# Kernel tuning notes

Measured on AMD Instinct MI355X. Metric: run time of the kernel, lower is better.

The kernel has to match this reference:

```python
import jax, jax.numpy as jnp
import numpy as np

BITS = 4
QMAX = 2 ** (BITS - 1) - 1   # 7
OFF = 2 ** (BITS - 1)        # 8
L = 2 ** BITS                # 16 LUT levels per operand


def _quant(x):
    """Symmetric per-tensor quantization to signed BITS-bit levels.
    Returns integer-valued levels (as float, in [-OFF, QMAX]) and the scale."""
    s = jnp.maximum(jnp.max(jnp.abs(x)) / QMAX, 1e-8)
    q = jnp.clip(jnp.round(x / s), -OFF, QMAX)
    return q, s


def _lut_conv3x3(x, w, b, lut):
    """3x3 same-padding conv where every scalar multiply a*w is replaced by
    lut[idx(a), idx(w)]. x:[B,C,H,W], w:[O,C,3,3], b:[O], lut:[L,L]."""
    B, C, H, W = x.shape
    O = w.shape[0]
    qx, sx = _quant(x)
    qw, sw = _quant(w)
    # zero-padding: level 0 is the quantized value 0, so padding is exact
    xp = jnp.pad(qx, ((0, 0), (0, 0), (1, 1), (1, 1)))
    # im2col: [B, C, 9, H, W] -> [B, H, W, K], K = C*9 (order: c-major, then kh,kw)
    patches = jnp.stack([xp[:, :, i:i + H, j:j + W]
                         for i in range(3) for j in range(3)], axis=2)
    K = C * 9
    patches = patches.reshape(B, K, H, W).transpose(0, 2, 3, 1)
    idx_a = (patches + OFF).astype(jnp.int32)            # [B,H,W,K]
    mapped = lut[idx_a]                                   # [B,H,W,K,L]
    idx_w = (qw.reshape(O, K).T + OFF).astype(jnp.int32)  # [K,O]
    onehot_w = jax.nn.one_hot(idx_w, L, dtype=x.dtype)    # [K,O,L]
    # out[b,o,h,w] = sum_k lut[idx_a[b,h,w,k], idx_w[k,o]]
    out = jnp.einsum('bhwkl,kol->bohw', mapped, onehot_w)
    return out * (sx * sw) + b[None, :, None, None]


def _lut_linear(x, w, b, lut):
    """x:[B,F], w:[O,F], b:[O], lut:[L,L]; y[b,o]=sum_f lut[idx(x),idx(w)]."""
    qx, sx = _quant(x)
    qw, sw = _quant(w)
    idx_a = (qx + OFF).astype(jnp.int32)                 # [B,F]
    mapped = lut[idx_a]                                   # [B,F,L]
    idx_w = (qw.T + OFF).astype(jnp.int32)                # [F,O]
    onehot_w = jax.nn.one_hot(idx_w, L, dtype=x.dtype)    # [F,O,L]
    out = jnp.einsum('bfl,fol->bo', mapped, onehot_w)
    return out * (sx * sw) + b[None, :]


def _maxpool2(x):
    B, C, H, W = x.shape
    return x.reshape(B, C, H // 2, 2, W // 2, 2).max(axis=(3, 5))


def setup_inputs() -> dict:
    key = jax.random.key(0)
    ks = jax.random.split(key, 20)
    d = {}
    d['x'] = jax.random.normal(ks[0], (8, 3, 32, 32), jnp.float32)
    conv_shapes = [(64, 3), (192, 64), (384, 192), (256, 384), (256, 256)]
    for i, (o, c) in enumerate(conv_shapes):
        d[f'w{i}'] = jax.random.normal(ks[1 + 2 * i], (o, c, 3, 3), jnp.float32) * 0.05
        d[f'b{i}'] = jax.random.normal(ks[2 + 2 * i], (o,), jnp.float32) * 0.01
    fc_shapes = [(4096, 4096), (4096, 4096), (10, 4096)]
    for j, (o, f) in enumerate(fc_shapes):
        d[f'w{5 + j}'] = jax.random.normal(ks[11 + 2 * j], (o, f), jnp.float32) * 0.02
        d[f'b{5 + j}'] = jax.random.normal(ks[12 + 2 * j], (o,), jnp.float32) * 0.01
    # per-layer approximate-multiplier LUTs: exact product of signed levels + error
    levels = jnp.arange(-OFF, OFF, dtype=jnp.float32)       # [-8..7]
    base = jnp.outer(levels, levels)                        # [16,16]
    noise = jax.random.normal(ks[17], (8, L, L), jnp.float32) * 0.25
    d['luts'] = base[None, :, :] + noise
    return d


def reference(x, w0, b0, w1, b1, w2, b2, w3, b3, w4, b4,
              w5, b5, w6, b6, w7, b7, luts):
    relu = jax.nn.relu
    h = relu(_lut_conv3x3(x, w0, b0, luts[0]))
    h = _maxpool2(h)                                  # [B,64,16,16]
    h = relu(_lut_conv3x3(h, w1, b1, luts[1]))
    h = _maxpool2(h)                                  # [B,192,8,8]
    h = relu(_lut_conv3x3(h, w2, b2, luts[2]))        # [B,384,8,8]
    h = relu(_lut_conv3x3(h, w3, b3, luts[3]))        # [B,256,8,8]
    h = relu(_lut_conv3x3(h, w4, b4, luts[4]))
    h = _maxpool2(h)                                  # [B,256,4,4]
    h = h.reshape(h.shape[0], 256 * 4 * 4)
    h = relu(_lut_linear(h, w5, b5, luts[5]))         # dropout = identity (eval)
    h = relu(_lut_linear(h, w6, b6, luts[6]))
    return _lut_linear(h, w7, b7, luts[7])            # [B,10]
```

## Files before the change

### kernel.cpp

```cpp
#include <hip/hip_runtime.h>
#include <stdint.h>


#define DI __device__ __forceinline__

constexpr size_t alup(size_t x){ return (x + 511) & ~(size_t)511; }
constexpr size_t O_SLOTS = 0;
constexpr size_t O_IA0 = 512;
constexpr size_t O_IA1 = alup(O_IA0 + 24576);
constexpr size_t O_IA2 = alup(O_IA1 + 131072);
constexpr size_t O_IA3 = alup(O_IA2 + 98304);
constexpr size_t O_IA4 = alup(O_IA3 + 196608);
constexpr size_t O_IA5 = alup(O_IA4 + 131072);
constexpr size_t O_IA6 = alup(O_IA5 + 32768);
constexpr size_t O_IA7 = alup(O_IA6 + 32768);
constexpr size_t O_WP0 = alup(O_IA7 + 32768);
constexpr size_t O_WP1 = alup(O_WP0 + 864);
constexpr size_t O_WP2 = alup(O_WP1 + 55296);
constexpr size_t O_WP3 = alup(O_WP2 + 331776);
constexpr size_t O_WP4 = alup(O_WP3 + 442368);
constexpr size_t O_A1  = alup(O_WP4 + 294912);
constexpr size_t O_A2  = alup(O_A1 + 1048576);
constexpr size_t O_A3  = alup(O_A2 + 786432);
constexpr size_t O_A4  = alup(O_A3 + 1572864);
constexpr size_t O_A5  = alup(O_A4 + 1048576);
constexpr size_t O_H5  = alup(O_A5 + 262144);
constexpr size_t O_H6  = alup(O_H5 + 262144);
constexpr size_t O_P   = alup(O_H6 + 262144);


DI double getscale(const double* slots, int i){ return fmax(slots[i] / 7.0, 1e-8); }
DI int quant_idx_r(double v, double r){
  double q = fmin(fmax(rint(v * r), -8.0), 7.0);
  return (int)q + 8;
}
DI void atomicMaxD(double* addr, double v){
  atomicMax((unsigned long long*)addr, (unsigned long long)__double_as_longlong(v));
}

__global__ void k_zero(double* slots){ if (threadIdx.x < 16) slots[threadIdx.x] = 0.0; }

__global__ __launch_bounds__(256) void k_zerobuf(double4* p, int n4){
  int i = blockIdx.x*256 + threadIdx.x;
  if (i < n4){ double4 z; z.x=z.y=z.z=z.w=0.0; p[i] = z; }
}

__global__ __launch_bounds__(256) void k_wmax(
    const float* w0, const float* w1, const float* w2, const float* w3, const float* w4,
    const float* w5, const float* w6, const float* w7, const float* x, double* slots)
{
  const int sizes[9] = {1728,110592,663552,884736,589824,16777216,16777216,40960,24576};
  const int cum[10]  = {0,1,5,26,53,71,583,1095,1097,1098};
  int bid = blockIdx.x;
  int seg = 0;
  #pragma unroll
  for (int s2 = 0; s2 < 9; ++s2) if (bid >= cum[s2+1]) seg = s2+1;
  const float* p;
  switch (seg){
    case 0: p = w0; break; case 1: p = w1; break; case 2: p = w2; break;
    case 3: p = w3; break; case 4: p = w4; break; case 5: p = w5; break;
    case 6: p = w6; break; case 7: p = w7; break; default: p = x; break;
  }
  int n = sizes[seg];
  long base = (long)(bid - cum[seg]) * 32768;
  float m = 0.f;
  for (long i = base + threadIdx.x * 4; i < base + 32768 && i < (long)n; i += 1024){
    float4 v = *(const float4*)(p + i);
    m = fmaxf(m, fmaxf(fmaxf(fabsf(v.x), fabsf(v.y)), fmaxf(fabsf(v.z), fabsf(v.w))));
  }
  #pragma unroll
  for (int off = 32; off; off >>= 1) m = fmaxf(m, __shfl_xor(m, off, 64));
  __shared__ float red[4];
  if ((threadIdx.x & 63) == 0) red[threadIdx.x >> 6] = m;
  __syncthreads();
  if (threadIdx.x == 0)
    atomicMaxD(&slots[seg], (double)fmaxf(fmaxf(red[0], red[1]), fmaxf(red[2], red[3])));
}

__global__ __launch_bounds__(256) void k_wq(
    const float* w0, const float* w1, const float* w2, const float* w3, const float* w4,
    const float* x, const double* slots, uint8_t* ws)
{
  int item = blockIdx.x * 256 + threadIdx.x;
  if (item < 281304){
    const float* w; uint32_t* wp; int K; int r; double s;
    if (item < 216)        { w=w0; wp=(uint32_t*)(ws+O_WP0); K=27;   r=item;        s=getscale(slots,0); }
    else if (item < 14040) { w=w1; wp=(uint32_t*)(ws+O_WP1); K=576;  r=item-216;    s=getscale(slots,1); }
    else if (item < 96984) { w=w2; wp=(uint32_t*)(ws+O_WP2); K=1728; r=item-14040;  s=getscale(slots,2); }
    else if (item < 207576){ w=w3; wp=(uint32_t*)(ws+O_WP3); K=3456; r=item-96984;  s=getscale(slots,3); }
    else                   { w=w4; wp=(uint32_t*)(ws+O_WP4); K=2304; r=item-207576; s=getscale(slots,4); }
    double rs = 1.0 / s;
    int og = r / K, k = r % K;
    uint32_t pack = 0;
    #pragma unroll
    for (int j = 0; j < 8; ++j){
      double wv = (double)w[(size_t)(og*8 + j)*K + k];
      pack |= (uint32_t)quant_idx_r(wv, rs) << (4*j);
    }
    wp[og*K + k] = pack;
  } else if (item < 287448){
    int i2 = item - 281304;
    double rs = 1.0 / getscale(slots, 8);
    uint32_t pack = 0;
    #pragma unroll
    for (int r2 = 0; r2 < 4; ++r2)
      pack |= (uint32_t)quant_idx_r((double)x[i2*4 + r2], rs) << (8*r2);
    ((uint32_t*)(ws + O_IA0))[i2] = pack;
  }
}

__global__ __launch_bounds__(256) void k_conv0(
    const uint8_t* __restrict__ ia0, const uint32_t* __restrict__ wp0,
    const float* __restrict__ lut_g, const float* __restrict__ bias,
    double* slots, double* __restrict__ a1)
{
  __shared__ float lutT[256];
  int tid = threadIdx.x;
  lutT[(tid & 15)*16 + (tid >> 4)] = lut_g[tid];
  __syncthreads();
  int b = blockIdx.x >> 6, o = blockIdx.x & 63;
  int yp = tid >> 4, xp = tid & 15;
  double scale = getscale(slots, 8) * getscale(slots, 0);
  double bo = (double)bias[o];
  double pool = 0.0;
  #pragma unroll
  for (int dy = 0; dy < 2; ++dy)
  #pragma unroll
  for (int dx = 0; dx < 2; ++dx){
    int y = yp*2 + dy, x2 = xp*2 + dx;
    double sum = 0.0;
    #pragma unroll
    for (int c = 0; c < 3; ++c)
      #pragma unroll
      for (int ty = 0; ty < 3; ++ty)
        #pragma unroll
        for (int tx = 0; tx < 3; ++tx){
          int yy = y + ty - 1, xx = x2 + tx - 1;
          int ia = 8;
          if (yy >= 0 && yy < 32 && xx >= 0 && xx < 32)
            ia = ia0[((b*3 + c)*32 + yy)*32 + xx];
          uint32_t sw = wp0[(o >> 3)*27 + c*9 + ty*3 + tx];
          int iw = (sw >> ((o & 7)*4)) & 15;
          sum += (double)lutT[iw*16 + ia];
        }
    pool = fmax(pool, fmax(sum*scale + bo, 0.0));
  }
  a1[((b*64 + o)*16 + yp)*16 + xp] = pool;
  double m = pool;
  #pragma unroll
  for (int off = 32; off; off >>= 1) m = fmax(m, __shfl_xor(m, off, 64));
  __shared__ double red[4];
  if ((tid & 63) == 0) red[tid >> 6] = m;
  __syncthreads();
  if (tid == 0) atomicMaxD(&slots[9], fmax(fmax(red[0],red[1]), fmax(red[2],red[3])));
}

template<int C, int O, int H, int W, int CT, int ROWS, int SP, int KSPAIRS>
__global__ __launch_bounds__(256) void k_conv(
    const uint8_t* __restrict__ iain, const uint32_t* __restrict__ wp,
    const float* __restrict__ lut_g, double* __restrict__ P)
{
  constexpr int KT = CT*9;
  constexpr int AW = W + 2, AH = ROWS + 2;
  __shared__ float lutT[256];
  __shared__ uint32_t wps[4*KT];
  __shared__ uint8_t acts[2*CT*AH*AW];
  int tid = threadIdx.x;
  int bx = blockIdx.x;
  int kp = bx % KSPAIRS; int rem = bx / KSPAIRS;
  int ob = rem % (O/16); rem /= (O/16);
  int sp = rem % SP; int b = rem / SP;
  lutT[(tid & 15)*16 + (tid >> 4)] = lut_g[tid];
  for (int i = tid; i < 4*KT; i += 256){
    int w2 = i / KT, k = i % KT;
    int ksub2 = w2 >> 1, og2 = w2 & 1;
    wps[i] = wp[(size_t)(ob*2 + og2)*(C*9) + (size_t)(kp*2 + ksub2)*KT + k];
  }
  constexpr int ATOT = 2*CT*AH*AW;
  int c0base = kp*2*CT;
  for (int i = tid; i < ATOT; i += 256){
    int ct2 = i / (AH*AW);
    int r  = (i / AW) % AH;
    int cc = i % AW;
    int y = sp*ROWS + r - 1, x2 = cc - 1;
    uint8_t v = 8;
    if (y >= 0 && y < H && x2 >= 0 && x2 < W)
      v = iain[(((size_t)b*C + c0base + ct2)*H + y)*W + x2];
    acts[i] = v;
  }
  __syncthreads();
  int wid = tid >> 6, lane = tid & 63;
  int ksub = wid >> 1, og = wid & 1;
  int ly = lane / W, lx = lane % W;
  double acc[8] = {0,0,0,0,0,0,0,0};
  const uint32_t* wrow = &wps[wid*KT];
  #pragma unroll 2
  for (int ct = 0; ct < CT; ++ct){
    int abase = ((ksub*CT + ct)*AH + ly)*AW + lx;
    #pragma unroll
    for (int ty = 0; ty < 3; ++ty)
    #pragma unroll
    for (int tx = 0; tx < 3; ++tx){
      int ia = acts[abase + ty*AW + tx];
      uint32_t sw = (uint32_t)__builtin_amdgcn_readfirstlane((int)wrow[ct*9 + ty*3 + tx]);
      #pragma unroll
      for (int j = 0; j < 8; ++j)
        acc[j] += (double)lutT[((sw >> (4*j)) & 15u)*16 + ia];
    }
  }
  int y = sp*ROWS + ly;
  int obase = ob*16 + og*8;
  #pragma unroll
  for (int j = 0; j < 8; ++j)
    atomicAdd(&P[(((size_t)b*O + obase + j)*H + y)*W + lx], acc[j]);
}

template<int O, int Hc, int Wc, bool POOL>
__global__ __launch_bounds__(256) void k_post(
    const double* __restrict__ P, const float* __restrict__ bias,
    double* __restrict__ aout, double* slots, int sx_slot, int sw_slot, int ma_slot)
{
  constexpr int Ho = POOL ? Hc/2 : Hc, Wo = POOL ? Wc/2 : Wc;
  int i = blockIdx.x*256 + threadIdx.x;
  int x2 = i % Wo, y = (i / Wo) % Ho, o = (i / (Wo*Ho)) % O, b = i / (Wo*Ho*O);
  double scale = getscale(slots, sx_slot) * getscale(slots, sw_slot);
  double bo = (double)bias[o];
  double res;
  if (POOL){
    double p = 0.0;
    #pragma unroll
    for (int dy = 0; dy < 2; ++dy)
    #pragma unroll
    for (int dx = 0; dx < 2; ++dx){
      double s = P[(((size_t)b*O + o)*Hc + y*2+dy)*Wc + x2*2+dx];
      p = fmax(p, fmax(s*scale + bo, 0.0));
    }
    res = p;
  } else {
    double s = P[(((size_t)b*O + o)*Hc + y)*Wc + x2];
    res = fmax(s*scale + bo, 0.0);
  }
  aout[i] = res;
  double m = res;
  #pragma unroll
  for (int off = 32; off; off >>= 1) m = fmax(m, __shfl_xor(m, off, 64));
  __shared__ double red[4];
  if ((threadIdx.x & 63) == 0) red[threadIdx.x >> 6] = m;
  __syncthreads();
  if (threadIdx.x == 0)
    atomicMaxD(&slots[ma_slot], fmax(fmax(red[0],red[1]), fmax(red[2],red[3])));
}

__global__ __launch_bounds__(256) void k_aq_conv(
    const double* __restrict__ in, uint8_t* __restrict__ out,
    const double* slots, int slot, int n)
{
  int i = blockIdx.x*256 + threadIdx.x;
  if (i >= n) return;
  double rs = 1.0 / getscale(slots, slot);
  out[i] = (uint8_t)quant_idx_r(in[i], rs);
}

__global__ __launch_bounds__(256) void k_aq_fc(
    const double* __restrict__ in, uint32_t* __restrict__ lo, uint32_t* __restrict__ hi,
    const double* slots, int slot)
{
  int f = blockIdx.x*256 + threadIdx.x;
  double rs = 1.0 / getscale(slots, slot);
  uint32_t l = 0, h = 0;
  #pragma unroll
  for (int b2 = 0; b2 < 4; ++b2) l |= (uint32_t)quant_idx_r(in[(size_t)b2*4096 + f], rs) << (8*b2);
  #pragma unroll
  for (int b2 = 4; b2 < 8; ++b2) h |= (uint32_t)quant_idx_r(in[(size_t)b2*4096 + f], rs) << (8*(b2-4));
  lo[f] = l; hi[f] = h;
}

template<bool RELU>
__global__ __launch_bounds__(256) void k_fc(
    const float* __restrict__ Wm, const float* __restrict__ bias,
    const uint32_t* __restrict__ ialo, const uint32_t* __restrict__ iahi,
    const float* __restrict__ lut_g, double* __restrict__ out,
    double* slots, int sx_slot, int sw_slot, int ma_slot)
{
  __shared__ float lutT[256];
  __shared__ uint32_t los[4096], his[4096];
  __shared__ double red[4];
  int tid = threadIdx.x;
  lutT[(tid & 15)*16 + (tid >> 4)] = lut_g[tid];
  for (int i = tid; i < 4096; i += 256){ los[i] = ialo[i]; his[i] = iahi[i]; }
  __syncthreads();
  double sw = getscale(slots, sw_slot);
  double rsw = 1.0 / sw;
  double scale = getscale(slots, sx_slot) * sw;
  int wid = tid >> 6, lane = tid & 63;
  int o = blockIdx.x*4 + wid;
  const float* wr = Wm + (size_t)o*4096;
  double acc[8] = {0,0,0,0,0,0,0,0};
  #pragma unroll 2
  for (int ch = 0; ch < 64; ++ch){
    int f = ch*64 + lane;
    double wv = (double)wr[f];
    unsigned iw = (unsigned)quant_idx_r(wv, rsw);
    const float* lrow = &lutT[iw << 4];
    uint32_t lo = los[f], hi = his[f];
    acc[0] += (double)lrow[lo & 255];         acc[1] += (double)lrow[(lo >> 8) & 255];
    acc[2] += (double)lrow[(lo >> 16) & 255]; acc[3] += (double)lrow[lo >> 24];
    acc[4] += (double)lrow[hi & 255];         acc[5] += (double)lrow[(hi >> 8) & 255];
    acc[6] += (double)lrow[(hi >> 16) & 255]; acc[7] += (double)lrow[hi >> 24];
  }
  #pragma unroll
  for (int off = 32; off; off >>= 1)
    #pragma unroll
    for (int b2 = 0; b2 < 8; ++b2) acc[b2] += __shfl_xor(acc[b2], off, 64);
  if (lane == 0){
    double m = 0.0;
    double bo = (double)bias[o];
    #pragma unroll
    for (int b2 = 0; b2 < 8; ++b2){
      double h = acc[b2]*scale + bo;
      if (RELU) h = fmax(h, 0.0);
      out[(size_t)b2*4096 + o] = h;
      m = fmax(m, fabs(h));
    }
    red[wid] = m;
  }
  __syncthreads();
  if (tid == 0)
    atomicMaxD(&slots[ma_slot], fmax(fmax(red[0],red[1]), fmax(red[2],red[3])));
}

__global__ __launch_bounds__(256) void k_fc7(
    const float* __restrict__ Wm, const float* __restrict__ bias,
    const uint32_t* __restrict__ ialo, const uint32_t* __restrict__ iahi,
    const float* __restrict__ lut_g, float* __restrict__ out, const double* slots)
{
  __shared__ float lutT[256];
  __shared__ uint32_t los[4096], his[4096];
  __shared__ double red[4][8];
  int tid = threadIdx.x;
  lutT[(tid & 15)*16 + (tid >> 4)] = lut_g[tid];
  for (int i = tid; i < 4096; i += 256){ los[i] = ialo[i]; his[i] = iahi[i]; }
  __syncthreads();
  double sw = getscale(slots, 7);
  double rsw = 1.0 / sw;
  double scale = getscale(slots, 15) * sw;
  int o = blockIdx.x;
  const float* wr = Wm + (size_t)o*4096;
  double acc[8] = {0,0,0,0,0,0,0,0};
  for (int ch = 0; ch < 16; ++ch){
    int f = ch*256 + tid;
    double wv = (double)wr[f];
    unsigned iw = (unsigned)quant_idx_r(wv, rsw);
    const float* lrow = &lutT[iw << 4];
    uint32_t lo = los[f], hi = his[f];
    acc[0] += (double)lrow[lo & 255];         acc[1] += (double)lrow[(lo >> 8) & 255];
    acc[2] += (double)lrow[(lo >> 16) & 255]; acc[3] += (double)lrow[lo >> 24];
    acc[4] += (double)lrow[hi & 255];         acc[5] += (double)lrow[(hi >> 8) & 255];
    acc[6] += (double)lrow[(hi >> 16) & 255]; acc[7] += (double)lrow[hi >> 24];
  }
  int wid = tid >> 6, lane = tid & 63;
  #pragma unroll
  for (int off = 32; off; off >>= 1)
    #pragma unroll
    for (int b2 = 0; b2 < 8; ++b2) acc[b2] += __shfl_xor(acc[b2], off, 64);
  if (lane == 0){
    #pragma unroll
    for (int b2 = 0; b2 < 8; ++b2) red[wid][b2] = acc[b2];
  }
  __syncthreads();
  if (tid < 8){
    double v = red[0][tid] + red[1][tid] + red[2][tid] + red[3][tid];
    out[tid*10 + o] = (float)(v*scale + (double)bias[o]);
  }
}

extern "C" void kernel_launch(void* const* d_in, const int* in_sizes, int n_in,
                              void* d_out, int out_size, void* d_ws, size_t ws_size,
                              hipStream_t stream)
{
  (void)in_sizes; (void)n_in; (void)out_size; (void)ws_size;
  const float* x  = (const float*)d_in[0];
  const float* w0 = (const float*)d_in[1];  const float* b0 = (const float*)d_in[2];
  const float* w1 = (const float*)d_in[3];  const float* b1 = (const float*)d_in[4];
  const float* w2 = (const float*)d_in[5];  const float* b2 = (const float*)d_in[6];
  const float* w3 = (const float*)d_in[7];  const float* b3 = (const float*)d_in[8];
  const float* w4 = (const float*)d_in[9];  const float* b4 = (const float*)d_in[10];
  const float* w5 = (const float*)d_in[11]; const float* b5 = (const float*)d_in[12];
  const float* w6 = (const float*)d_in[13]; const float* b6 = (const float*)d_in[14];
  const float* w7 = (const float*)d_in[15]; const float* b7 = (const float*)d_in[16];
  const float* luts = (const float*)d_in[17];

  uint8_t* ws = (uint8_t*)d_ws;
  double* slots = (double*)(ws + O_SLOTS);
  const uint8_t* IA0 = ws + O_IA0;
  uint8_t *IA1 = ws + O_IA1, *IA2 = ws + O_IA2, *IA3 = ws + O_IA3, *IA4 = ws + O_IA4;
  uint32_t *IA5lo = (uint32_t*)(ws + O_IA5), *IA5hi = IA5lo + 4096;
  uint32_t *IA6lo = (uint32_t*)(ws + O_IA6), *IA6hi = IA6lo + 4096;
  uint32_t *IA7lo = (uint32_t*)(ws + O_IA7), *IA7hi = IA7lo + 4096;
  const uint32_t* WP0 = (const uint32_t*)(ws + O_WP0);
  const uint32_t* WP1 = (const uint32_t*)(ws + O_WP1);
  const uint32_t* WP2 = (const uint32_t*)(ws + O_WP2);
  const uint32_t* WP3 = (const uint32_t*)(ws + O_WP3);
  const uint32_t* WP4 = (const uint32_t*)(ws + O_WP4);
  double *A1 = (double*)(ws + O_A1), *A2 = (double*)(ws + O_A2), *A3 = (double*)(ws + O_A3);
  double *A4 = (double*)(ws + O_A4), *A5 = (double*)(ws + O_A5);
  double *H5 = (double*)(ws + O_H5), *H6 = (double*)(ws + O_H6);
  double *P = (double*)(ws + O_P);

  k_zero<<<1, 64, 0, stream>>>(slots);
  k_wmax<<<1098, 256, 0, stream>>>(w0,w1,w2,w3,w4,w5,w6,w7,x,slots);
  k_wq<<<1123, 256, 0, stream>>>(w0,w1,w2,w3,w4,x,slots,ws);

  k_conv0<<<512, 256, 0, stream>>>(IA0, WP0, luts + 0, b0, slots, A1);
  k_aq_conv<<<512, 256, 0, stream>>>(A1, IA1, slots, 9, 131072);

  k_zerobuf<<<384, 256, 0, stream>>>((double4*)P, 98304);
  k_conv<64,192,16,16,8,4,4,4><<<1536, 256, 0, stream>>>(IA1, WP1, luts + 256, P);
  k_post<192,16,16,true><<<384, 256, 0, stream>>>(P, b1, A2, slots, 9, 1, 10);
  k_aq_conv<<<384, 256, 0, stream>>>(A2, IA2, slots, 10, 98304);

  k_zerobuf<<<192, 256, 0, stream>>>((double4*)P, 49152);
  k_conv<192,384,8,8,12,8,1,8><<<1536, 256, 0, stream>>>(IA2, WP2, luts + 512, P);
  k_post<384,8,8,false><<<768, 256, 0, stream>>>(P, b2, A3, slots, 10, 2, 11);
  k_aq_conv<<<768, 256, 0, stream>>>(A3, IA3, slots, 11, 196608);

  k_zerobuf<<<128, 256, 0, stream>>>((double4*)P, 32768);
  k_conv<384,256,8,8,16,8,1,12><<<1536, 256, 0, stream>>>(IA3, WP3, luts + 768, P);
  k_post<256,8,8,false><<<512, 256, 0, stream>>>(P, b3, A4, slots, 11, 3, 12);
  k_aq_conv<<<512, 256, 0, stream>>>(A4, IA4, slots, 12, 131072);

  k_zerobuf<<<128, 256, 0, stream>>>((double4*)P, 32768);
  k_conv<256,256,8,8,8,8,1,16><<<2048, 256, 0, stream>>>(IA4, WP4, luts + 1024, P);
  k_post<256,8,8,true><<<128, 256, 0, stream>>>(P, b4, A5, slots, 12, 4, 13);
  k_aq_fc<<<16, 256, 0, stream>>>(A5, IA5lo, IA5hi, slots, 13);

  k_fc<true><<<1024, 256, 0, stream>>>(w5, b5, IA5lo, IA5hi, luts + 1280, H5, slots, 13, 5, 14);
  k_aq_fc<<<16, 256, 0, stream>>>(H5, IA6lo, IA6hi, slots, 14);
  k_fc<true><<<1024, 256, 0, stream>>>(w6, b6, IA6lo, IA6hi, luts + 1536, H6, slots, 14, 6, 15);
  k_aq_fc<<<16, 256, 0, stream>>>(H6, IA7lo, IA7hi, slots, 15);
  k_fc7<<<10, 256, 0, stream>>>(w7, b7, IA7lo, IA7hi, luts + 1792, (float*)d_out, slots);
}
```

Measured before the change: 529.9 us.

## Pack two batch activations per byte and use paired LUT lookups

Builds a 4096-entry float2 pair table so a single LDS lookup indexed by weight level and a packed pair of activation codes returns the LUT values for two batch elements at once. Conv and FC kernels now process all batch pairs within one block, with activations repacked two per byte. Separate per-layer partial buffers are all zeroed in one upfront kernel, which removes the per-layer zerobuf launches. The cost is a larger LDS table build per block and a different conv split and tiling, which changes occupancy and atomic contention.

```diff
diff --git a/kernel.cpp b/kernel.cpp
--- a/kernel.cpp
+++ b/kernel.cpp
@@ -8,13 +8,13 @@
 constexpr size_t O_SLOTS = 0;
 constexpr size_t O_IA0 = 512;
 constexpr size_t O_IA1 = alup(O_IA0 + 24576);
-constexpr size_t O_IA2 = alup(O_IA1 + 131072);
-constexpr size_t O_IA3 = alup(O_IA2 + 98304);
-constexpr size_t O_IA4 = alup(O_IA3 + 196608);
-constexpr size_t O_IA5 = alup(O_IA4 + 131072);
-constexpr size_t O_IA6 = alup(O_IA5 + 32768);
-constexpr size_t O_IA7 = alup(O_IA6 + 32768);
-constexpr size_t O_WP0 = alup(O_IA7 + 32768);
+constexpr size_t O_IA2 = alup(O_IA1 + 65536);
+constexpr size_t O_IA3 = alup(O_IA2 + 49152);
+constexpr size_t O_IA4 = alup(O_IA3 + 98304);
+constexpr size_t O_IA5 = alup(O_IA4 + 65536);
+constexpr size_t O_IA6 = alup(O_IA5 + 16384);
+constexpr size_t O_IA7 = alup(O_IA6 + 16384);
+constexpr size_t O_WP0 = alup(O_IA7 + 16384);
 constexpr size_t O_WP1 = alup(O_WP0 + 864);
 constexpr size_t O_WP2 = alup(O_WP1 + 55296);
 constexpr size_t O_WP3 = alup(O_WP2 + 331776);
@@ -27,6 +27,11 @@
 constexpr size_t O_H5  = alup(O_A5 + 262144);
 constexpr size_t O_H6  = alup(O_H5 + 262144);
 constexpr size_t O_P   = alup(O_H6 + 262144);
+constexpr size_t O_P1  = O_P;
+constexpr size_t O_P2  = O_P1 + 3145728;
+constexpr size_t O_P3  = O_P2 + 1572864;
+constexpr size_t O_P4  = O_P3 + 1048576;
+constexpr int    PZ_D4 = 212992;
 
 
 DI double getscale(const double* slots, int i){ return fmax(slots[i] / 7.0, 1e-8); }
@@ -38,11 +43,10 @@
   atomicMax((unsigned long long*)addr, (unsigned long long)__double_as_longlong(v));
 }
 
-__global__ void k_zero(double* slots){ if (threadIdx.x < 16) slots[threadIdx.x] = 0.0; }
-
-__global__ __launch_bounds__(256) void k_zerobuf(double4* p, int n4){
+__global__ __launch_bounds__(256) void k_zero_all(double4* pz, double* slots){
   int i = blockIdx.x*256 + threadIdx.x;
-  if (i < n4){ double4 z; z.x=z.y=z.z=z.w=0.0; p[i] = z; }
+  if (i < PZ_D4){ double4 z; z.x=z.y=z.z=z.w=0.0; pz[i] = z; }
+  else if (i - PZ_D4 < 16) slots[i - PZ_D4] = 0.0;
 }
 
 __global__ __launch_bounds__(256) void k_wmax(
@@ -155,64 +159,67 @@
   if (tid == 0) atomicMaxD(&slots[9], fmax(fmax(red[0],red[1]), fmax(red[2],red[3])));
 }
 
-template<int C, int O, int H, int W, int CT, int ROWS, int SP, int KSPAIRS>
-__global__ __launch_bounds__(256) void k_conv(
+template<int C, int O, int H, int W, int CT, int ROWS, int SP, int KS>
+__global__ __launch_bounds__(256) void k_convP(
     const uint8_t* __restrict__ iain, const uint32_t* __restrict__ wp,
     const float* __restrict__ lut_g, double* __restrict__ P)
 {
-  constexpr int KT = CT*9;
   constexpr int AW = W + 2, AH = ROWS + 2;
-  __shared__ float lutT[256];
-  __shared__ uint32_t wps[4*KT];
-  __shared__ uint8_t acts[2*CT*AH*AW];
+  __shared__ float2 pairT[4096];
+  __shared__ uint32_t wps[CT*9];
+  __shared__ uint8_t actsC[4*CT*AH*AW];
   int tid = threadIdx.x;
   int bx = blockIdx.x;
-  int kp = bx % KSPAIRS; int rem = bx / KSPAIRS;
-  int ob = rem % (O/16); rem /= (O/16);
-  int sp = rem % SP; int b = rem / SP;
-  lutT[(tid & 15)*16 + (tid >> 4)] = lut_g[tid];
-  for (int i = tid; i < 4*KT; i += 256){
-    int w2 = i / KT, k = i % KT;
-    int ksub2 = w2 >> 1, og2 = w2 & 1;
-    wps[i] = wp[(size_t)(ob*2 + og2)*(C*9) + (size_t)(kp*2 + ksub2)*KT + k];
-  }
-  constexpr int ATOT = 2*CT*AH*AW;
-  int c0base = kp*2*CT;
+  int ks = bx % KS; int rem = bx / KS;
+  int ob = rem % (O/8); int sp = rem / (O/8);
+  for (int e = tid; e < 4096; e += 256){
+    int iw = e >> 8, a1 = (e >> 4) & 15, a2 = e & 15;
+    pairT[e] = make_float2(lut_g[a1*16 + iw], lut_g[a2*16 + iw]);
+  }
+  for (int i = tid; i < CT*9; i += 256)
+    wps[i] = wp[(size_t)ob*(C*9) + ks*CT*9 + i];
+  constexpr int ATOT = 4*CT*AH*AW;
   for (int i = tid; i < ATOT; i += 256){
-    int ct2 = i / (AH*AW);
-    int r  = (i / AW) % AH;
-    int cc = i % AW;
+    int p2 = i / (CT*AH*AW);
+    int r2 = i % (CT*AH*AW);
+    int ct = r2 / (AH*AW);
+    int r = (r2 / AW) % AH;
+    int cc = r2 % AW;
     int y = sp*ROWS + r - 1, x2 = cc - 1;
-    uint8_t v = 8;
+    uint8_t v = 136;
     if (y >= 0 && y < H && x2 >= 0 && x2 < W)
-      v = iain[(((size_t)b*C + c0base + ct2)*H + y)*W + x2];
-    acts[i] = v;
-  }
-  __syncthreads();
-  int wid = tid >> 6, lane = tid & 63;
-  int ksub = wid >> 1, og = wid & 1;
+      v = iain[(((size_t)p2*C + ks*CT + ct)*H + y)*W + x2];
+    actsC[i] = v;
+  }
+  __syncthreads();
+  int p = tid >> 6, lane = tid & 63;
   int ly = lane / W, lx = lane % W;
-  double acc[8] = {0,0,0,0,0,0,0,0};
-  const uint32_t* wrow = &wps[wid*KT];
-  #pragma unroll 2
+  double acc0[8] = {0,0,0,0,0,0,0,0};
+  double acc1[8] = {0,0,0,0,0,0,0,0};
+  #pragma unroll 1
   for (int ct = 0; ct < CT; ++ct){
-    int abase = ((ksub*CT + ct)*AH + ly)*AW + lx;
+    int abase = ((p*CT + ct)*AH + ly)*AW + lx;
     #pragma unroll
     for (int ty = 0; ty < 3; ++ty)
     #pragma unroll
     for (int tx = 0; tx < 3; ++tx){
-      int ia = acts[abase + ty*AW + tx];
-      uint32_t sw = (uint32_t)__builtin_amdgcn_readfirstlane((int)wrow[ct*9 + ty*3 + tx]);
+      int c = actsC[abase + ty*AW + tx];
+      uint32_t sw = (uint32_t)__builtin_amdgcn_readfirstlane((int)wps[ct*9 + ty*3 + tx]);
       #pragma unroll
-      for (int j = 0; j < 8; ++j)
-        acc[j] += (double)lutT[((sw >> (4*j)) & 15u)*16 + ia];
+      for (int j = 0; j < 8; ++j){
+        float2 v = pairT[(((sw >> (4*j)) & 15u) << 8) + c];
+        acc0[j] += (double)v.x;
+        acc1[j] += (double)v.y;
+      }
     }
   }
   int y = sp*ROWS + ly;
-  int obase = ob*16 + og*8;
-  #pragma unroll
-  for (int j = 0; j < 8; ++j)
-    atomicAdd(&P[(((size_t)b*O + obase + j)*H + y)*W + lx], acc[j]);
+  #pragma unroll
+  for (int j = 0; j < 8; ++j){
+    size_t base = (((size_t)(2*p)*O + ob*8 + j)*H + y)*W + lx;
+    atomicAdd(&P[base], acc0[j]);
+    atomicAdd(&P[base + (size_t)O*H*W], acc1[j]);
+  }
 }
 
 template<int O, int Hc, int Wc, bool POOL>
@@ -251,43 +258,50 @@
     atomicMaxD(&slots[ma_slot], fmax(fmax(red[0],red[1]), fmax(red[2],red[3])));
 }
 
-__global__ __launch_bounds__(256) void k_aq_conv(
+__global__ __launch_bounds__(256) void k_aq_convP(
     const double* __restrict__ in, uint8_t* __restrict__ out,
-    const double* slots, int slot, int n)
+    const double* slots, int slot, int CHW, int n)
 {
   int i = blockIdx.x*256 + threadIdx.x;
   if (i >= n) return;
   double rs = 1.0 / getscale(slots, slot);
-  out[i] = (uint8_t)quant_idx_r(in[i], rs);
-}
-
-__global__ __launch_bounds__(256) void k_aq_fc(
-    const double* __restrict__ in, uint32_t* __restrict__ lo, uint32_t* __restrict__ hi,
+  int p = i / CHW, rr = i % CHW;
+  int q1 = quant_idx_r(in[(size_t)(2*p)*CHW + rr], rs);
+  int q2 = quant_idx_r(in[(size_t)(2*p+1)*CHW + rr], rs);
+  out[i] = (uint8_t)((q1 << 4) | q2);
+}
+
+__global__ __launch_bounds__(256) void k_aq_fcP(
+    const double* __restrict__ in, uint32_t* __restrict__ cmb,
     const double* slots, int slot)
 {
   int f = blockIdx.x*256 + threadIdx.x;
   double rs = 1.0 / getscale(slots, slot);
-  uint32_t l = 0, h = 0;
-  #pragma unroll
-  for (int b2 = 0; b2 < 4; ++b2) l |= (uint32_t)quant_idx_r(in[(size_t)b2*4096 + f], rs) << (8*b2);
-  #pragma unroll
-  for (int b2 = 4; b2 < 8; ++b2) h |= (uint32_t)quant_idx_r(in[(size_t)b2*4096 + f], rs) << (8*(b2-4));
-  lo[f] = l; hi[f] = h;
+  uint32_t r = 0;
+  #pragma unroll
+  for (int p = 0; p < 4; ++p){
+    int q1 = quant_idx_r(in[(size_t)(2*p)*4096 + f], rs);
+    int q2 = quant_idx_r(in[(size_t)(2*p+1)*4096 + f], rs);
+    r |= (uint32_t)((q1 << 4) | q2) << (8*p);
+  }
+  cmb[f] = r;
 }
 
 template<bool RELU>
-__global__ __launch_bounds__(256) void k_fc(
+__global__ __launch_bounds__(256) void k_fcP(
     const float* __restrict__ Wm, const float* __restrict__ bias,
-    const uint32_t* __restrict__ ialo, const uint32_t* __restrict__ iahi,
-    const float* __restrict__ lut_g, double* __restrict__ out,
-    double* slots, int sx_slot, int sw_slot, int ma_slot)
-{
-  __shared__ float lutT[256];
-  __shared__ uint32_t los[4096], his[4096];
+    const uint32_t* __restrict__ cmb, const float* __restrict__ lut_g,
+    double* __restrict__ out, double* slots, int sx_slot, int sw_slot, int ma_slot)
+{
+  __shared__ float2 pairT[4096];
+  __shared__ uint32_t cmbS[4096];
   __shared__ double red[4];
   int tid = threadIdx.x;
-  lutT[(tid & 15)*16 + (tid >> 4)] = lut_g[tid];
-  for (int i = tid; i < 4096; i += 256){ los[i] = ialo[i]; his[i] = iahi[i]; }
+  for (int e = tid; e < 4096; e += 256){
+    int iw = e >> 8, a1 = (e >> 4) & 15, a2 = e & 15;
+    pairT[e] = make_float2(lut_g[a1*16 + iw], lut_g[a2*16 + iw]);
+  }
+  for (int i = tid; i < 4096; i += 256) cmbS[i] = cmb[i];
   __syncthreads();
   double sw = getscale(slots, sw_slot);
   double rsw = 1.0 / sw;
@@ -299,14 +313,13 @@
   #pragma unroll 2
   for (int ch = 0; ch < 64; ++ch){
     int f = ch*64 + lane;
-    double wv = (double)wr[f];
-    unsigned iw = (unsigned)quant_idx_r(wv, rsw);
-    const float* lrow = &lutT[iw << 4];
-    uint32_t lo = los[f], hi = his[f];
-    acc[0] += (double)lrow[lo & 255];         acc[1] += (double)lrow[(lo >> 8) & 255];
-    acc[2] += (double)lrow[(lo >> 16) & 255]; acc[3] += (double)lrow[lo >> 24];
-    acc[4] += (double)lrow[hi & 255];         acc[5] += (double)lrow[(hi >> 8) & 255];
-    acc[6] += (double)lrow[(hi >> 16) & 255]; acc[7] += (double)lrow[hi >> 24];
+    unsigned iw = (unsigned)quant_idx_r((double)wr[f], rsw);
+    const float2* row = &pairT[iw << 8];
+    uint32_t cb = cmbS[f];
+    float2 v0 = row[cb & 255];         acc[0] += (double)v0.x; acc[1] += (double)v0.y;
+    float2 v1 = row[(cb >> 8) & 255];  acc[2] += (double)v1.x; acc[3] += (double)v1.y;
+    float2 v2 = row[(cb >> 16) & 255]; acc[4] += (double)v2.x; acc[5] += (double)v2.y;
+    float2 v3 = row[cb >> 24];         acc[6] += (double)v3.x; acc[7] += (double)v3.y;
   }
   #pragma unroll
   for (int off = 32; off; off >>= 1)
@@ -329,17 +342,20 @@
     atomicMaxD(&slots[ma_slot], fmax(fmax(red[0],red[1]), fmax(red[2],red[3])));
 }
 
-__global__ __launch_bounds__(256) void k_fc7(
+__global__ __launch_bounds__(256) void k_fc7P(
     const float* __restrict__ Wm, const float* __restrict__ bias,
-    const uint32_t* __restrict__ ialo, const uint32_t* __restrict__ iahi,
-    const float* __restrict__ lut_g, float* __restrict__ out, const double* slots)
-{
-  __shared__ float lutT[256];
-  __shared__ uint32_t los[4096], his[4096];
+    const uint32_t* __restrict__ cmb, const float* __restrict__ lut_g,
+    float* __restrict__ out, const double* slots)
+{
+  __shared__ float2 pairT[4096];
+  __shared__ uint32_t cmbS[4096];
   __shared__ double red[4][8];
   int tid = threadIdx.x;
-  lutT[(tid & 15)*16 + (tid >> 4)] = lut_g[tid];
-  for (int i = tid; i < 4096; i += 256){ los[i] = ialo[i]; his[i] = iahi[i]; }
+  for (int e = tid; e < 4096; e += 256){
+    int iw = e >> 8, a1 = (e >> 4) & 15, a2 = e & 15;
+    pairT[e] = make_float2(lut_g[a1*16 + iw], lut_g[a2*16 + iw]);
+  }
+  for (int i = tid; i < 4096; i += 256) cmbS[i] = cmb[i];
   __syncthreads();
   double sw = getscale(slots, 7);
   double rsw = 1.0 / sw;
@@ -349,14 +365,13 @@
   double acc[8] = {0,0,0,0,0,0,0,0};
   for (int ch = 0; ch < 16; ++ch){
     int f = ch*256 + tid;
-    double wv = (double)wr[f];
-    unsigned iw = (unsigned)quant_idx_r(wv, rsw);
-    const float* lrow = &lutT[iw << 4];
-    uint32_t lo = los[f], hi = his[f];
-    acc[0] += (double)lrow[lo & 255];         acc[1] += (double)lrow[(lo >> 8) & 255];
-    acc[2] += (double)lrow[(lo >> 16) & 255]; acc[3] += (double)lrow[lo >> 24];
-    acc[4] += (double)lrow[hi & 255];         acc[5] += (double)lrow[(hi >> 8) & 255];
-    acc[6] += (double)lrow[(hi >> 16) & 255]; acc[7] += (double)lrow[hi >> 24];
+    unsigned iw = (unsigned)quant_idx_r((double)wr[f], rsw);
+    const float2* row = &pairT[iw << 8];
+    uint32_t cb = cmbS[f];
+    float2 v0 = row[cb & 255];         acc[0] += (double)v0.x; acc[1] += (double)v0.y;
+    float2 v1 = row[(cb >> 8) & 255];  acc[2] += (double)v1.x; acc[3] += (double)v1.y;
+    float2 v2 = row[(cb >> 16) & 255]; acc[4] += (double)v2.x; acc[5] += (double)v2.y;
+    float2 v3 = row[cb >> 24];         acc[6] += (double)v3.x; acc[7] += (double)v3.y;
   }
   int wid = tid >> 6, lane = tid & 63;
   #pragma unroll
@@ -394,9 +409,9 @@
   double* slots = (double*)(ws + O_SLOTS);
   const uint8_t* IA0 = ws + O_IA0;
   uint8_t *IA1 = ws + O_IA1, *IA2 = ws + O_IA2, *IA3 = ws + O_IA3, *IA4 = ws + O_IA4;
-  uint32_t *IA5lo = (uint32_t*)(ws + O_IA5), *IA5hi = IA5lo + 4096;
-  uint32_t *IA6lo = (uint32_t*)(ws + O_IA6), *IA6hi = IA6lo + 4096;
-  uint32_t *IA7lo = (uint32_t*)(ws + O_IA7), *IA7hi = IA7lo + 4096;
+  uint32_t *IA5 = (uint32_t*)(ws + O_IA5);
+  uint32_t *IA6 = (uint32_t*)(ws + O_IA6);
+  uint32_t *IA7 = (uint32_t*)(ws + O_IA7);
   const uint32_t* WP0 = (const uint32_t*)(ws + O_WP0);
   const uint32_t* WP1 = (const uint32_t*)(ws + O_WP1);
   const uint32_t* WP2 = (const uint32_t*)(ws + O_WP2);
@@ -405,38 +420,35 @@
   double *A1 = (double*)(ws + O_A1), *A2 = (double*)(ws + O_A2), *A3 = (double*)(ws + O_A3);
   double *A4 = (double*)(ws + O_A4), *A5 = (double*)(ws + O_A5);
   double *H5 = (double*)(ws + O_H5), *H6 = (double*)(ws + O_H6);
-  double *P = (double*)(ws + O_P);
-
-  k_zero<<<1, 64, 0, stream>>>(slots);
+  double *P1 = (double*)(ws + O_P1), *P2 = (double*)(ws + O_P2);
+  double *P3 = (double*)(ws + O_P3), *P4 = (double*)(ws + O_P4);
+
+  k_zero_all<<<833, 256, 0, stream>>>((double4*)(ws + O_P), slots);
   k_wmax<<<1098, 256, 0, stream>>>(w0,w1,w2,w3,w4,w5,w6,w7,x,slots);
   k_wq<<<1123, 256, 0, stream>>>(w0,w1,w2,w3,w4,x,slots,ws);
 
   k_conv0<<<512, 256, 0, stream>>>(IA0, WP0, luts + 0, b0, slots, A1);
-  k_aq_conv<<<512, 256, 0, stream>>>(A1, IA1, slots, 9, 131072);
-
-  k_zerobuf<<<384, 256, 0, stream>>>((double4*)P, 98304);
-  k_conv<64,192,16,16,8,4,4,4><<<1536, 256, 0, stream>>>(IA1, WP1, luts + 256, P);
-  k_post<192,16,16,true><<<384, 256, 0, stream>>>(P, b1, A2, slots, 9, 1, 10);
-  k_aq_conv<<<384, 256, 0, stream>>>(A2, IA2, slots, 10, 98304);
-
-  k_zerobuf<<<192, 256, 0, stream>>>((double4*)P, 49152);
-  k_conv<192,384,8,8,12,8,1,8><<<1536, 256, 0, stream>>>(IA2, WP2, luts + 512, P);
-  k_post<384,8,8,false><<<768, 256, 0, stream>>>(P, b2, A3, slots, 10, 2, 11);
-  k_aq_conv<<<768, 256, 0, stream>>>(A3, IA3, slots, 11, 196608);
-
-  k_zerobuf<<<128, 256, 0, stream>>>((double4*)P, 32768);
-  k_conv<384,256,8,8,16,8,1,12><<<1536, 256, 0, stream>>>(IA3, WP3, luts + 768, P);
-  k_post<256,8,8,false><<<512, 256, 0, stream>>>(P, b3, A4, slots, 11, 3, 12);
-  k_aq_conv<<<512, 256, 0, stream>>>(A4, IA4, slots, 12, 131072);
-
-  k_zerobuf<<<128, 256, 0, stream>>>((double4*)P, 32768);
-  k_conv<256,256,8,8,8,8,1,16><<<2048, 256, 0, stream>>>(IA4, WP4, luts + 1024, P);
-  k_post<256,8,8,true><<<128, 256, 0, stream>>>(P, b4, A5, slots, 12, 4, 13);
-  k_aq_fc<<<16, 256, 0, stream>>>(A5, IA5lo, IA5hi, slots, 13);
-
-  k_fc<true><<<1024, 256, 0, stream>>>(w5, b5, IA5lo, IA5hi, luts + 1280, H5, slots, 13, 5, 14);
-  k_aq_fc<<<16, 256, 0, stream>>>(H5, IA6lo, IA6hi, slots, 14);
-  k_fc<true><<<1024, 256, 0, stream>>>(w6, b6, IA6lo, IA6hi, luts + 1536, H6, slots, 14, 6, 15);
-  k_aq_fc<<<16, 256, 0, stream>>>(H6, IA7lo, IA7hi, slots, 15);
-  k_fc7<<<10, 256, 0, stream>>>(w7, b7, IA7lo, IA7hi, luts + 1792, (float*)d_out, slots);
-}
+  k_aq_convP<<<256, 256, 0, stream>>>(A1, IA1, slots, 9, 16384, 65536);
+
+  k_convP<64,192,16,16,8,4,4,8><<<768, 256, 0, stream>>>(IA1, WP1, luts + 256, P1);
+  k_post<192,16,16,true><<<384, 256, 0, stream>>>(P1, b1, A2, slots, 9, 1, 10);
+  k_aq_convP<<<192, 256, 0, stream>>>(A2, IA2, slots, 10, 12288, 49152);
+
+  k_convP<192,384,8,8,8,8,1,24><<<1152, 256, 0, stream>>>(IA2, WP2, luts + 512, P2);
+  k_post<384,8,8,false><<<768, 256, 0, stream>>>(P2, b2, A3, slots, 10, 2, 11);
+  k_aq_convP<<<384, 256, 0, stream>>>(A3, IA3, slots, 11, 24576, 98304);
+
+  k_convP<384,256,8,8,12,8,1,32><<<1024, 256, 0, stream>>>(IA3, WP3, luts + 768, P3);
+  k_post<256,8,8,false><<<512, 256, 0, stream>>>(P3, b3, A4, slots, 11, 3, 12);
+  k_aq_convP<<<256, 256, 0, stream>>>(A4, IA4, slots, 12, 16384, 65536);
+
+  k_convP<256,256,8,8,8,8,1,32><<<1024, 256, 0, stream>>>(IA4, WP4, luts + 1024, P4);
+  k_post<256,8,8,true><<<128, 256, 0, stream>>>(P4, b4, A5, slots, 12, 4, 13);
+  k_aq_fcP<<<16, 256, 0, stream>>>(A5, IA5, slots, 13);
+
+  k_fcP<true><<<1024, 256, 0, stream>>>(w5, b5, IA5, luts + 1280, H5, slots, 13, 5, 14);
+  k_aq_fcP<<<16, 256, 0, stream>>>(H5, IA6, slots, 14);
+  k_fcP<true><<<1024, 256, 0, stream>>>(w6, b6, IA6, luts + 1536, H6, slots, 14, 6, 15);
+  k_aq_fcP<<<16, 256, 0, stream>>>(H6, IA7, slots, 15);
+  k_fc7P<<<10, 256, 0, stream>>>(w7, b7, IA7, luts + 1792, (float*)d_out, slots);
+}
```

Result: slower. 592.5 us (+11.8%).

## Retile LUT conv blocks by output channels, store LUTs as double, merge zeroing

Applied to the files above, without the earlier changes.

Conv blocks now have each of four wavefronts handle a different group of 8 output channels over one shared K-slice, instead of pairing two K-subslices with two output groups. This halves the activation tile each block stages and doubles the K-split count. LUTs are held in shared memory as double, so the per-lookup float-to-double conversion goes away at the cost of wider LDS reads. The per-layer partial buffers are separated and zeroed, together with the scale slots, in a single up-front kernel that replaces several small zeroing launches, which uses more workspace memory. The extra K-splits also mean more atomic adds into those partial buffers.

```diff
diff --git a/kernel.cpp b/kernel.cpp
--- a/kernel.cpp
+++ b/kernel.cpp
@@ -26,7 +26,11 @@
 constexpr size_t O_A5  = alup(O_A4 + 1048576);
 constexpr size_t O_H5  = alup(O_A5 + 262144);
 constexpr size_t O_H6  = alup(O_H5 + 262144);
-constexpr size_t O_P   = alup(O_H6 + 262144);
+constexpr size_t O_P1  = alup(O_H6 + 262144);
+constexpr size_t O_P2  = O_P1 + 3145728;
+constexpr size_t O_P3  = O_P2 + 1572864;
+constexpr size_t O_P4  = O_P3 + 1048576;
+constexpr int    PZ_D4 = 212992;
 
 
 DI double getscale(const double* slots, int i){ return fmax(slots[i] / 7.0, 1e-8); }
@@ -38,11 +42,10 @@
   atomicMax((unsigned long long*)addr, (unsigned long long)__double_as_longlong(v));
 }
 
-__global__ void k_zero(double* slots){ if (threadIdx.x < 16) slots[threadIdx.x] = 0.0; }
-
-__global__ __launch_bounds__(256) void k_zerobuf(double4* p, int n4){
+__global__ __launch_bounds__(256) void k_zero_all(double4* pz, double* slots){
   int i = blockIdx.x*256 + threadIdx.x;
-  if (i < n4){ double4 z; z.x=z.y=z.z=z.w=0.0; p[i] = z; }
+  if (i < PZ_D4){ double4 z; z.x=z.y=z.z=z.w=0.0; pz[i] = z; }
+  else if (i - PZ_D4 < 16) slots[i - PZ_D4] = 0.0;
 }
 
 __global__ __launch_bounds__(256) void k_wmax(
@@ -114,9 +117,9 @@
     const float* __restrict__ lut_g, const float* __restrict__ bias,
     double* slots, double* __restrict__ a1)
 {
-  __shared__ float lutT[256];
+  __shared__ double lutT[256];
   int tid = threadIdx.x;
-  lutT[(tid & 15)*16 + (tid >> 4)] = lut_g[tid];
+  lutT[(tid & 15)*16 + (tid >> 4)] = (double)lut_g[tid];
   __syncthreads();
   int b = blockIdx.x >> 6, o = blockIdx.x & 63;
   int yp = tid >> 4, xp = tid & 15;
@@ -141,7 +144,7 @@
             ia = ia0[((b*3 + c)*32 + yy)*32 + xx];
           uint32_t sw = wp0[(o >> 3)*27 + c*9 + ty*3 + tx];
           int iw = (sw >> ((o & 7)*4)) & 15;
-          sum += (double)lutT[iw*16 + ia];
+          sum += lutT[iw*16 + ia];
         }
     pool = fmax(pool, fmax(sum*scale + bo, 0.0));
   }
@@ -155,48 +158,44 @@
   if (tid == 0) atomicMaxD(&slots[9], fmax(fmax(red[0],red[1]), fmax(red[2],red[3])));
 }
 
-template<int C, int O, int H, int W, int CT, int ROWS, int SP, int KSPAIRS>
+template<int C, int O, int H, int W, int CT, int ROWS, int SP, int KS>
 __global__ __launch_bounds__(256) void k_conv(
     const uint8_t* __restrict__ iain, const uint32_t* __restrict__ wp,
     const float* __restrict__ lut_g, double* __restrict__ P)
 {
   constexpr int KT = CT*9;
   constexpr int AW = W + 2, AH = ROWS + 2;
-  __shared__ float lutT[256];
+  __shared__ double lutT[256];
   __shared__ uint32_t wps[4*KT];
-  __shared__ uint8_t acts[2*CT*AH*AW];
+  __shared__ uint8_t acts[CT*AH*AW];
   int tid = threadIdx.x;
   int bx = blockIdx.x;
-  int kp = bx % KSPAIRS; int rem = bx / KSPAIRS;
-  int ob = rem % (O/16); rem /= (O/16);
+  int ks = bx % KS; int rem = bx / KS;
+  int ob = rem % (O/32); rem /= (O/32);
   int sp = rem % SP; int b = rem / SP;
-  lutT[(tid & 15)*16 + (tid >> 4)] = lut_g[tid];
+  lutT[(tid & 15)*16 + (tid >> 4)] = (double)lut_g[tid];
   for (int i = tid; i < 4*KT; i += 256){
     int w2 = i / KT, k = i % KT;
-    int ksub2 = w2 >> 1, og2 = w2 & 1;
-    wps[i] = wp[(size_t)(ob*2 + og2)*(C*9) + (size_t)(kp*2 + ksub2)*KT + k];
-  }
-  constexpr int ATOT = 2*CT*AH*AW;
-  int c0base = kp*2*CT;
-  for (int i = tid; i < ATOT; i += 256){
-    int ct2 = i / (AH*AW);
+    wps[i] = wp[(size_t)(ob*4 + w2)*(C*9) + (size_t)ks*KT + k];
+  }
+  for (int i = tid; i < CT*AH*AW; i += 256){
+    int ct = i / (AH*AW);
     int r  = (i / AW) % AH;
     int cc = i % AW;
     int y = sp*ROWS + r - 1, x2 = cc - 1;
     uint8_t v = 8;
     if (y >= 0 && y < H && x2 >= 0 && x2 < W)
-      v = iain[(((size_t)b*C + c0base + ct2)*H + y)*W + x2];
+      v = iain[(((size_t)b*C + ks*CT + ct)*H + y)*W + x2];
     acts[i] = v;
   }
   __syncthreads();
   int wid = tid >> 6, lane = tid & 63;
-  int ksub = wid >> 1, og = wid & 1;
   int ly = lane / W, lx = lane % W;
   double acc[8] = {0,0,0,0,0,0,0,0};
   const uint32_t* wrow = &wps[wid*KT];
-  #pragma unroll 2
+  #pragma unroll 1
   for (int ct = 0; ct < CT; ++ct){
-    int abase = ((ksub*CT + ct)*AH + ly)*AW + lx;
+    int abase = (ct*AH + ly)*AW + lx;
     #pragma unroll
     for (int ty = 0; ty < 3; ++ty)
     #pragma unroll
@@ -205,11 +204,11 @@
       uint32_t sw = (uint32_t)__builtin_amdgcn_readfirstlane((int)wrow[ct*9 + ty*3 + tx]);
       #pragma unroll
       for (int j = 0; j < 8; ++j)
-        acc[j] += (double)lutT[((sw >> (4*j)) & 15u)*16 + ia];
+        acc[j] += lutT[((sw >> (4*j)) & 15u)*16 + ia];
     }
   }
   int y = sp*ROWS + ly;
-  int obase = ob*16 + og*8;
+  int obase = ob*32 + wid*8;
   #pragma unroll
   for (int j = 0; j < 8; ++j)
     atomicAdd(&P[(((size_t)b*O + obase + j)*H + y)*W + lx], acc[j]);
@@ -282,11 +281,11 @@
     const float* __restrict__ lut_g, double* __restrict__ out,
     double* slots, int sx_slot, int sw_slot, int ma_slot)
 {
-  __shared__ float lutT[256];
+  __shared__ double lutT[256];
   __shared__ uint32_t los[4096], his[4096];
   __shared__ double red[4];
   int tid = threadIdx.x;
-  lutT[(tid & 15)*16 + (tid >> 4)] = lut_g[tid];
+  lutT[(tid & 15)*16 + (tid >> 4)] = (double)lut_g[tid];
   for (int i = tid; i < 4096; i += 256){ los[i] = ialo[i]; his[i] = iahi[i]; }
   __syncthreads();
   double sw = getscale(slots, sw_slot);
@@ -299,14 +298,13 @@
   #pragma unroll 2
   for (int ch = 0; ch < 64; ++ch){
     int f = ch*64 + lane;
-    double wv = (double)wr[f];
-    unsigned iw = (unsigned)quant_idx_r(wv, rsw);
-    const float* lrow = &lutT[iw << 4];
+    unsigned iw = (unsigned)quant_idx_r((double)wr[f], rsw);
+    const double* lrow = &lutT[iw << 4];
     uint32_t lo = los[f], hi = his[f];
-    acc[0] += (double)lrow[lo & 255];         acc[1] += (double)lrow[(lo >> 8) & 255];
-    acc[2] += (double)lrow[(lo >> 16) & 255]; acc[3] += (double)lrow[lo >> 24];
-    acc[4] += (double)lrow[hi & 255];         acc[5] += (double)lrow[(hi >> 8) & 255];
-    acc[6] += (double)lrow[(hi >> 16) & 255]; acc[7] += (double)lrow[hi >> 24];
+    acc[0] += lrow[lo & 255];         acc[1] += lrow[(lo >> 8) & 255];
+    acc[2] += lrow[(lo >> 16) & 255]; acc[3] += lrow[lo >> 24];
+    acc[4] += lrow[hi & 255];         acc[5] += lrow[(hi >> 8) & 255];
+    acc[6] += lrow[(hi >> 16) & 255]; acc[7] += lrow[hi >> 24];
   }
   #pragma unroll
   for (int off = 32; off; off >>= 1)
@@ -334,11 +332,11 @@
     const uint32_t* __restrict__ ialo, const uint32_t* __restrict__ iahi,
     const float* __restrict__ lut_g, float* __restrict__ out, const double* slots)
 {
-  __shared__ float lutT[256];
+  __shared__ double lutT[256];
   __shared__ uint32_t los[4096], his[4096];
   __shared__ double red[4][8];
   int tid = threadIdx.x;
-  lutT[(tid & 15)*16 + (tid >> 4)] = lut_g[tid];
+  lutT[(tid & 15)*16 + (tid >> 4)] = (double)lut_g[tid];
   for (int i = tid; i < 4096; i += 256){ los[i] = ialo[i]; his[i] = iahi[i]; }
   __syncthreads();
   double sw = getscale(slots, 7);
@@ -349,14 +347,13 @@
   double acc[8] = {0,0,0,0,0,0,0,0};
   for (int ch = 0; ch < 16; ++ch){
     int f = ch*256 + tid;
-    double wv = (double)wr[f];
-    unsigned iw = (unsigned)quant_idx_r(wv, rsw);
-    const float* lrow = &lutT[iw << 4];
+    unsigned iw = (unsigned)quant_idx_r((double)wr[f], rsw);
+    const double* lrow = &lutT[iw << 4];
     uint32_t lo = los[f], hi = his[f];
-    acc[0] += (double)lrow[lo & 255];         acc[1] += (double)lrow[(lo >> 8) & 255];
-    acc[2] += (double)lrow[(lo >> 16) & 255]; acc[3] += (double)lrow[lo >> 24];
-    acc[4] += (double)lrow[hi & 255];         acc[5] += (double)lrow[(hi >> 8) & 255];
-    acc[6] += (double)lrow[(hi >> 16) & 255]; acc[7] += (double)lrow[hi >> 24];
+    acc[0] += lrow[lo & 255];         acc[1] += lrow[(lo >> 8) & 255];
+    acc[2] += lrow[(lo >> 16) & 255]; acc[3] += lrow[lo >> 24];
+    acc[4] += lrow[hi & 255];         acc[5] += lrow[(hi >> 8) & 255];
+    acc[6] += lrow[(hi >> 16) & 255]; acc[7] += lrow[hi >> 24];
   }
   int wid = tid >> 6, lane = tid & 63;
   #pragma unroll
@@ -405,33 +402,30 @@
   double *A1 = (double*)(ws + O_A1), *A2 = (double*)(ws + O_A2), *A3 = (double*)(ws + O_A3);
   double *A4 = (double*)(ws + O_A4), *A5 = (double*)(ws + O_A5);
   double *H5 = (double*)(ws + O_H5), *H6 = (double*)(ws + O_H6);
-  double *P = (double*)(ws + O_P);
-
-  k_zero<<<1, 64, 0, stream>>>(slots);
+  double *P1 = (double*)(ws + O_P1), *P2 = (double*)(ws + O_P2);
+  double *P3 = (double*)(ws + O_P3), *P4 = (double*)(ws + O_P4);
+
+  k_zero_all<<<833, 256, 0, stream>>>((double4*)(ws + O_P1), slots);
   k_wmax<<<1098, 256, 0, stream>>>(w0,w1,w2,w3,w4,w5,w6,w7,x,slots);
   k_wq<<<1123, 256, 0, stream>>>(w0,w1,w2,w3,w4,x,slots,ws);
 
   k_conv0<<<512, 256, 0, stream>>>(IA0, WP0, luts + 0, b0, slots, A1);
   k_aq_conv<<<512, 256, 0, stream>>>(A1, IA1, slots, 9, 131072);
 
-  k_zerobuf<<<384, 256, 0, stream>>>((double4*)P, 98304);
-  k_conv<64,192,16,16,8,4,4,4><<<1536, 256, 0, stream>>>(IA1, WP1, luts + 256, P);
-  k_post<192,16,16,true><<<384, 256, 0, stream>>>(P, b1, A2, slots, 9, 1, 10);
+  k_conv<64,192,16,16,8,4,4,8><<<1536, 256, 0, stream>>>(IA1, WP1, luts + 256, P1);
+  k_post<192,16,16,true><<<384, 256, 0, stream>>>(P1, b1, A2, slots, 9, 1, 10);
   k_aq_conv<<<384, 256, 0, stream>>>(A2, IA2, slots, 10, 98304);
 
-  k_zerobuf<<<192, 256, 0, stream>>>((double4*)P, 49152);
-  k_conv<192,384,8,8,12,8,1,8><<<1536, 256, 0, stream>>>(IA2, WP2, luts + 512, P);
-  k_post<384,8,8,false><<<768, 256, 0, stream>>>(P, b2, A3, slots, 10, 2, 11);
+  k_conv<192,384,8,8,12,8,1,16><<<1536, 256, 0, stream>>>(IA2, WP2, luts + 512, P2);
+  k_post<384,8,8,false><<<768, 256, 0, stream>>>(P2, b2, A3, slots, 10, 2, 11);
   k_aq_conv<<<768, 256, 0, stream>>>(A3, IA3, slots, 11, 196608);
 
-  k_zerobuf<<<128, 256, 0, stream>>>((double4*)P, 32768);
-  k_conv<384,256,8,8,16,8,1,12><<<1536, 256, 0, stream>>>(IA3, WP3, luts + 768, P);
-  k_post<256,8,8,false><<<512, 256, 0, stream>>>(P, b3, A4, slots, 11, 3, 12);
+  k_conv<384,256,8,8,12,8,1,32><<<2048, 256, 0, stream>>>(IA3, WP3, luts + 768, P3);
+  k_post<256,8,8,false><<<512, 256, 0, stream>>>(P3, b3, A4, slots, 11, 3, 12);
   k_aq_conv<<<512, 256, 0, stream>>>(A4, IA4, slots, 12, 131072);
 
-  k_zerobuf<<<128, 256, 0, stream>>>((double4*)P, 32768);
-  k_conv<256,256,8,8,8,8,1,16><<<2048, 256, 0, stream>>>(IA4, WP4, luts + 1024, P);
-  k_post<256,8,8,true><<<128, 256, 0, stream>>>(P, b4, A5, slots, 12, 4, 13);
+  k_conv<256,256,8,8,8,8,1,32><<<2048, 256, 0, stream>>>(IA4, WP4, luts + 1024, P4);
+  k_post<256,8,8,true><<<128, 256, 0, stream>>>(P4, b4, A5, slots, 12, 4, 13);
   k_aq_fc<<<16, 256, 0, stream>>>(A5, IA5lo, IA5hi, slots, 13);
 
   k_fc<true><<<1024, 256, 0, stream>>>(w5, b5, IA5lo, IA5hi, luts + 1280, H5, slots, 13, 5, 14);
```

New measurement: 503.0 us. 5.1% less time.
